# Kernel tuning notes

Measured on AMD Instinct MI355X. Metric: run time of the kernel, lower is better.

Reference implementation:

```python
import jax, jax.numpy as jnp
import numpy as np

D_MODEL = 768
NHEAD = 12
DK = D_MODEL // NHEAD
MAX_DIST = 1000.0
FF = 3072
POS_HIDDEN = 32  # hidden width of the relative-position bias MLP
EPS = 1e-5
B, L = 2, 1024


def setup_inputs() -> dict:
    key = jax.random.key(0)
    ks = jax.random.split(key, 24)

    def lin(k, i, o):  # torch-Linear-like init, stored as (in, out)
        return jax.random.uniform(k, (i, o), jnp.float32, -1.0, 1.0) / np.sqrt(i)

    return {
        "src": jax.random.normal(ks[0], (B, L, D_MODEL), jnp.float32),
        "src_x": jax.random.uniform(ks[1], (B, L), jnp.float32) * 1000.0,
        "src_y": jax.random.uniform(ks[2], (B, L), jnp.float32) * 1000.0,
        # attention projections (q,k,v,out)
        "Wq": lin(ks[3], D_MODEL, D_MODEL), "bq": jnp.zeros((D_MODEL,), jnp.float32),
        "Wk": lin(ks[4], D_MODEL, D_MODEL), "bk": jnp.zeros((D_MODEL,), jnp.float32),
        "Wv": lin(ks[5], D_MODEL, D_MODEL), "bv": jnp.zeros((D_MODEL,), jnp.float32),
        "Wo": lin(ks[6], D_MODEL, D_MODEL), "bo": jnp.zeros((D_MODEL,), jnp.float32),
        # relative-position bias MLP: 2 -> POS_HIDDEN -> NHEAD
        "P1": lin(ks[7], 2, POS_HIDDEN), "pb1": jnp.zeros((POS_HIDDEN,), jnp.float32),
        "P2": lin(ks[8], POS_HIDDEN, NHEAD), "pb2": jnp.zeros((NHEAD,), jnp.float32),
        # FFN
        "W1": lin(ks[9], D_MODEL, FF), "b1": jnp.zeros((FF,), jnp.float32),
        "W2": lin(ks[10], FF, D_MODEL), "b2": jnp.zeros((D_MODEL,), jnp.float32),
        # post-LN params
        "g1": jnp.ones((D_MODEL,), jnp.float32), "be1": jnp.zeros((D_MODEL,), jnp.float32),
        "g2": jnp.ones((D_MODEL,), jnp.float32), "be2": jnp.zeros((D_MODEL,), jnp.float32),
    }


def _layernorm(x, g, b):
    m = jnp.mean(x, axis=-1, keepdims=True)
    v = jnp.var(x, axis=-1, keepdims=True)
    return (x - m) * jax.lax.rsqrt(v + EPS) * g + b


def reference(src, src_x, src_y, Wq, bq, Wk, bk, Wv, bv, Wo, bo,
              P1, pb1, P2, pb2, W1, b1, W2, b2, g1, be1, g2, be2):
    b, l, _ = src.shape
    # projections -> (b, h, l, dk)
    q = (src @ Wq + bq).reshape(b, l, NHEAD, DK).transpose(0, 2, 1, 3)
    k = (src @ Wk + bk).reshape(b, l, NHEAD, DK).transpose(0, 2, 1, 3)
    v = (src @ Wv + bv).reshape(b, l, NHEAD, DK).transpose(0, 2, 1, 3)
    # 2D relative positions, clipped and normalized to [-1, 1]
    rx = jnp.clip(src_x[:, :, None] - src_x[:, None, :], -MAX_DIST, MAX_DIST) / MAX_DIST
    ry = jnp.clip(src_y[:, :, None] - src_y[:, None, :], -MAX_DIST, MAX_DIST) / MAX_DIST
    rel = jnp.stack([rx, ry], axis=-1)                        # (b, l, l, 2)
    bias = jax.nn.relu(rel @ P1 + pb1) @ P2 + pb2             # (b, l, l, h)
    bias = bias.transpose(0, 3, 1, 2)                         # (b, h, l, l)
    scores = jnp.einsum('bhqd,bhkd->bhqk', q, k) / np.sqrt(DK).astype(np.float32) + bias
    attn = jax.nn.softmax(scores, axis=-1)
    o = jnp.einsum('bhqk,bhkd->bhqd', attn, v).transpose(0, 2, 1, 3).reshape(b, l, D_MODEL)
    src2 = o @ Wo + bo
    x = _layernorm(src + src2, g1, be1)                       # post-LN residual 1
    ff = jax.nn.relu(x @ W1 + b1) @ W2 + b2                   # FFN
    return _layernorm(x + ff, g2, be2)                        # post-LN residual 2
```

## Files before the change

kernel.cpp:

```cpp
#include <hip/hip_runtime.h>
#include <math.h>

typedef unsigned short ushort_t;
typedef __attribute__((ext_vector_type(8))) short bf16x8;
typedef __attribute__((ext_vector_type(4))) float f32x4;

constexpr int kD      = 768;
constexpr int kNH     = 12;
constexpr int kDK     = 64;
constexpr int kFF     = 3072;
constexpr int kL      = 1024;
constexpr int kRows   = 2048;
constexpr float kEPS  = 1e-5f;
constexpr int kMLRows = 24 * kL;

__device__ __forceinline__ ushort_t f2bf(float f) {
    union { float f; unsigned u; } v; v.f = f;
    unsigned r = (v.u + 0x7fffu + ((v.u >> 16) & 1u)) >> 16;
    return (ushort_t)r;
}
__device__ __forceinline__ float bf2f(ushort_t u) {
    union { unsigned u; float f; } v; v.u = ((unsigned)u) << 16; return v.f;
}

#define GL_LDS(gp, lp) __builtin_amdgcn_global_load_lds( \
    (const __attribute__((address_space(1))) void*)(gp), \
    (__attribute__((address_space(3))) void*)(lp), 16, 0, 0)

template<int RELU, int OUTBF, int ADDBIAS>
__device__ __forceinline__ void gemm_body(const ushort_t* __restrict__ A,
                                          const ushort_t* __restrict__ WT,
                                          const float* __restrict__ bias,
                                          void* __restrict__ Cout,
                                          int N, int K, int row0, int col0,
                                          int kbeg, int kend)
{
    __shared__ ushort_t lds[8192];
    ushort_t* As = lds;
    ushort_t* Bs = lds + 4096;

    const int tid  = threadIdx.x;
    const int lane = tid & 63;
    const int wave = tid >> 6;
    const int wrow = (wave & 1) * 64;
    const int wcol = (wave >> 1) * 64;

    const int srow = wave * 16 + (lane >> 2);
    const int sk   = (lane & 3) * 8;
    const ushort_t* ga0 = A  + (size_t)(row0 + srow)      * K + sk;
    const ushort_t* ga1 = A  + (size_t)(row0 + srow + 64) * K + sk;
    const ushort_t* gb0 = WT + (size_t)(col0 + srow)      * K + sk;
    const ushort_t* gb1 = WT + (size_t)(col0 + srow + 64) * K + sk;
    ushort_t* la0 = As + wave * 512;
    ushort_t* la1 = As + 2048 + wave * 512;
    ushort_t* lb0 = Bs + wave * 512;
    ushort_t* lb1 = Bs + 2048 + wave * 512;

    const int fl = lane & 15, fq = lane >> 4;
    const ushort_t* fa[4];
    const ushort_t* fb[4];
    #pragma unroll
    for (int i = 0; i < 4; ++i) {
        fa[i] = As + (wrow + i * 16 + fl) * 32 + fq * 8;
        fb[i] = Bs + (wcol + i * 16 + fl) * 32 + fq * 8;
    }

    f32x4 acc[4][4] = {};

    for (int k0 = kbeg; k0 < kend; k0 += 32) {
        __syncthreads();
        GL_LDS(ga0 + k0, la0);
        GL_LDS(ga1 + k0, la1);
        GL_LDS(gb0 + k0, lb0);
        GL_LDS(gb1 + k0, lb1);
        __syncthreads();

        bf16x8 av[4], bv[4];
        #pragma unroll
        for (int i = 0; i < 4; ++i) {
            av[i] = *(const bf16x8*)fa[i];
            bv[i] = *(const bf16x8*)fb[i];
        }
        #pragma unroll
        for (int mi = 0; mi < 4; ++mi)
            #pragma unroll
            for (int ni = 0; ni < 4; ++ni)
                acc[mi][ni] = __builtin_amdgcn_mfma_f32_16x16x32_bf16(
                    av[mi], bv[ni], acc[mi][ni], 0, 0, 0);
    }

    #pragma unroll
    for (int mi = 0; mi < 4; ++mi) {
        const int m = wrow + mi * 16 + fq * 4;
        #pragma unroll
        for (int ni = 0; ni < 4; ++ni) {
            const int n = wcol + ni * 16 + fl;
            const float bb = ADDBIAS ? bias[col0 + n] : 0.f;
            #pragma unroll
            for (int r = 0; r < 4; ++r) {
                float v = acc[mi][ni][r] + bb;
                if (RELU) v = fmaxf(v, 0.f);
                const size_t idx = (size_t)(row0 + m + r) * N + col0 + n;
                if (OUTBF) ((ushort_t*)Cout)[idx] = f2bf(v);
                else       ((float*)Cout)[idx]    = v;
            }
        }
    }
}

template<int RELU, int OUTBF>
__global__ __launch_bounds__(256)
void gemm_kernel(const ushort_t* __restrict__ A, const ushort_t* __restrict__ WT,
                 const float* __restrict__ bias, void* __restrict__ Cout,
                 int N, int K)
{
    gemm_body<RELU, OUTBF, 1>(A, WT, bias, Cout, N, K,
                              blockIdx.y * 128, blockIdx.x * 128, 0, K);
}

__global__ __launch_bounds__(256)
void gemm_splitk_kernel(const ushort_t* __restrict__ A, const ushort_t* __restrict__ WT,
                        float* __restrict__ parts, int N, int K, int kslice)
{
    const int z = blockIdx.z;
    float* out = parts + (size_t)z * kRows * N;
    gemm_body<0, 0, 0>(A, WT, nullptr, out, N, K,
                       blockIdx.y * 128, blockIdx.x * 128, z * kslice, (z + 1) * kslice);
}

__global__ __launch_bounds__(256)
void gemm_qkv_kernel(const ushort_t* __restrict__ A,
                     const ushort_t* wq, const ushort_t* wk, const ushort_t* wv,
                     const float* bq, const float* bk, const float* bv,
                     ushort_t* q, ushort_t* k, ushort_t* v)
{
    const ushort_t* WT; const float* bias; ushort_t* out;
    if (blockIdx.z == 0)      { WT = wq; bias = bq; out = q; }
    else if (blockIdx.z == 1) { WT = wk; bias = bk; out = k; }
    else                      { WT = wv; bias = bv; out = v; }
    gemm_body<0, 1, 1>(A, WT, bias, out, kD, kD,
                       blockIdx.y * 128, blockIdx.x * 128, 0, kD);
}

struct WtDesc { const float* src; ushort_t* dst; int K; int N; };
struct WtArgs { WtDesc d[3]; };

__global__ __launch_bounds__(256)
void wt_kernel(WtArgs args)
{
    const WtDesc w = args.d[blockIdx.z];
    const int ktiles = w.K >> 6;
    const int kt = (blockIdx.x % ktiles) * 64;
    const int nt = (blockIdx.x / ktiles) * 64;
    if (nt >= w.N) return;

    __shared__ float T[64][65];
    const int tid = threadIdx.x;
    #pragma unroll
    for (int i = 0; i < 4; ++i) {
        const int e = tid + i * 256;
        const int r = e >> 4;
        const int c = (e & 15) * 4;
        const float4 f = *(const float4*)&w.src[(size_t)(kt + r) * w.N + nt + c];
        T[c + 0][r] = f.x; T[c + 1][r] = f.y; T[c + 2][r] = f.z; T[c + 3][r] = f.w;
    }
    __syncthreads();
    #pragma unroll
    for (int i = 0; i < 4; ++i) {
        const int e = tid + i * 256;
        const int n = e >> 4;
        const int kc = (e & 15) * 4;
        ushort4 o;
        o.x = f2bf(T[n][kc + 0]); o.y = f2bf(T[n][kc + 1]);
        o.z = f2bf(T[n][kc + 2]); o.w = f2bf(T[n][kc + 3]);
        *(ushort4*)&w.dst[(size_t)(nt + n) * w.K + kt + kc] = o;
    }
}

__global__ __launch_bounds__(256)
void cvt_kernel(const float* __restrict__ in, ushort_t* __restrict__ out, int n4)
{
    const int i = blockIdx.x * 256 + threadIdx.x;
    if (i < n4) {
        const float4 f = ((const float4*)in)[i];
        ushort4 o;
        o.x = f2bf(f.x); o.y = f2bf(f.y); o.z = f2bf(f.z); o.w = f2bf(f.w);
        ((ushort4*)out)[i] = o;
    }
}

__global__ __launch_bounds__(256)
void vtrans_kernel(const ushort_t* __restrict__ vb, ushort_t* __restrict__ vt)
{
    const int bh = blockIdx.x;
    const int b = bh / kNH, h = bh - b * kNH;
    const int j0 = blockIdx.y * 64;
    __shared__ ushort_t T[64][72];

    const int tid = threadIdx.x;
    {
        const int jr = tid & 63;
        const int c0 = (tid >> 6) * 16;
        const ushort_t* sp = vb + (size_t)(b * kL + j0 + jr) * kD + h * kDK + c0;
        uint4 u0 = *(const uint4*)sp;
        uint4 u1 = *(const uint4*)(sp + 8);
        const ushort_t* e0 = (const ushort_t*)&u0;
        const ushort_t* e1 = (const ushort_t*)&u1;
        #pragma unroll
        for (int jj = 0; jj < 8; ++jj) {
            T[c0 + jj][jr]     = e0[jj];
            T[c0 + 8 + jj][jr] = e1[jj];
        }
    }
    __syncthreads();
    {
        const int dr = tid >> 2;
        const int jc = (tid & 3) * 16;
        ushort_t* dp = vt + (size_t)(bh * 64 + dr) * kL + j0 + jc;
        *(uint4*)dp       = *(const uint4*)&T[dr][jc];
        *(uint4*)(dp + 8) = *(const uint4*)&T[dr][jc + 8];
    }
}

__global__ __launch_bounds__(256, 4)
void bias_kernel(const float* __restrict__ sx, const float* __restrict__ sy,
                 const float* __restrict__ P1, const float* __restrict__ pb1,
                 const float* __restrict__ P2, const float* __restrict__ pb2,
                 ushort_t* __restrict__ biasb)
{
    const int bid = blockIdx.x;
    const int b  = bid >> 10;
    const int qt = (bid >> 4) & 63;
    const int kt = bid & 15;
    const int tid = threadIdx.x;

    __shared__ float P[32][16];
    __shared__ float pb2l[12];
    __shared__ float qxl[16], qyl[16], kxl[64], kyl[64];
    __shared__ ushort_t Btile[12 * 1024];

    if (tid < 32) {
        P[tid][0] = P1[tid];
        P[tid][1] = P1[32 + tid];
        P[tid][2] = pb1[tid];
        P[tid][3] = 0.f;
    }
    for (int e = tid; e < 384; e += 256) P[e / 12][4 + e % 12] = P2[e];
    if (tid < 12) pb2l[tid] = pb2[tid];
    if (tid < 16) { qxl[tid] = sx[b * kL + qt * 16 + tid];
                    qyl[tid] = sy[b * kL + qt * 16 + tid]; }
    if (tid < 64) { kxl[tid] = sx[b * kL + kt * 64 + tid];
                    kyl[tid] = sy[b * kL + kt * 64 + tid]; }
    __syncthreads();

    const int ri = tid >> 4;
    const int fl = tid & 15;
    const int fq = ri >> 2, r = ri & 3;
    const int lane16 = fq * 16 + fl;
    const float xi = qxl[ri], yi = qyl[ri];

    float rx[4], ry[4];
    #pragma unroll
    for (int n = 0; n < 4; ++n) {
        const int cj = n * 16 + fl;
        rx[n] = fminf(fmaxf(xi - kxl[cj], -1000.f), 1000.f) * 1e-3f;
        ry[n] = fminf(fmaxf(yi - kyl[cj], -1000.f), 1000.f) * 1e-3f;
    }

    float acc[4][12] = {};
    #pragma unroll 4
    for (int u = 0; u < 32; ++u) {
        const float4 pc = *(const float4*)&P[u][0];
        const float4 w0 = *(const float4*)&P[u][4];
        const float4 w1 = *(const float4*)&P[u][8];
        const float4 w2 = *(const float4*)&P[u][12];
        float t[4];
        #pragma unroll
        for (int n = 0; n < 4; ++n)
            t[n] = fmaxf(fmaf(rx[n], pc.x, fmaf(ry[n], pc.y, pc.z)), 0.f);
        #pragma unroll
        for (int n = 0; n < 4; ++n) {
            acc[n][0]  = fmaf(t[n], w0.x, acc[n][0]);
            acc[n][1]  = fmaf(t[n], w0.y, acc[n][1]);
            acc[n][2]  = fmaf(t[n], w0.z, acc[n][2]);
            acc[n][3]  = fmaf(t[n], w0.w, acc[n][3]);
            acc[n][4]  = fmaf(t[n], w1.x, acc[n][4]);
            acc[n][5]  = fmaf(t[n], w1.y, acc[n][5]);
            acc[n][6]  = fmaf(t[n], w1.z, acc[n][6]);
            acc[n][7]  = fmaf(t[n], w1.w, acc[n][7]);
            acc[n][8]  = fmaf(t[n], w2.x, acc[n][8]);
            acc[n][9]  = fmaf(t[n], w2.y, acc[n][9]);
            acc[n][10] = fmaf(t[n], w2.z, acc[n][10]);
            acc[n][11] = fmaf(t[n], w2.w, acc[n][11]);
        }
    }

    #pragma unroll
    for (int h = 0; h < 12; ++h) {
        const float pb = pb2l[h];
        #pragma unroll
        for (int n = 0; n < 4; ++n)
            Btile[h * 1024 + lane16 * 16 + n * 4 + r] = f2bf(acc[n][h] + pb);
    }
    __syncthreads();

    #pragma unroll
    for (int i = 0; i < 6; ++i) {
        const int off = (i * 256 + tid) * 8;
        const int h = off >> 10;
        const int inner = off & 1023;
        ushort_t* dst = biasb +
            (((size_t)(b * kNH + h) * 64 + qt) * 16 + kt) * 1024 + inner;
        *(uint4*)dst = *(const uint4*)&Btile[off];
    }
}

__global__ __launch_bounds__(64, 3)
void attn_kernel(const ushort_t* __restrict__ qg, const ushort_t* __restrict__ kg,
                 const ushort_t* __restrict__ vt, const ushort_t* __restrict__ biasb,
                 ushort_t* __restrict__ p0, ushort_t* __restrict__ p1,
                 ushort_t* __restrict__ p2, ushort_t* __restrict__ p3,
                 float2* __restrict__ ml)
{
    const int bh = blockIdx.x;
    const int b  = bh / kNH, h = bh - b * kNH;
    const int qt = blockIdx.y;
    const int q0 = qt * 16;
    const int z  = blockIdx.z;
    const int lane = threadIdx.x;
    const int fl = lane & 15, fq = lane >> 4;

    __shared__ ushort_t Sp[16][72];

    const size_t qoff = (size_t)(b * kL + q0 + fl) * kD + h * kDK + fq * 8;
    const bf16x8 aq0 = *(const bf16x8*)(qg + qoff);
    const bf16x8 aq1 = *(const bf16x8*)(qg + qoff + 32);

    const ushort_t* kbase = kg + (size_t)(b * kL) * kD + h * kDK + fq * 8;
    const ushort_t* vbase = vt + (size_t)(bh * 64) * kL + fq * 8;
    const ushort_t* btile = biasb +
        ((size_t)(bh * 64 + qt) * 16 + z * 4) * 1024 + lane * 16;

    f32x4 accO[4] = {};
    float m_run[4] = {-INFINITY, -INFINITY, -INFINITY, -INFINITY};
    float l_run[4] = {};

    bf16x8 kc[4][2];
    uint4 bc0, bc1;
    {
        const int k0 = z * 256;
        #pragma unroll
        for (int n = 0; n < 4; ++n) {
            const ushort_t* kr = kbase + (size_t)(k0 + n * 16 + fl) * kD;
            kc[n][0] = *(const bf16x8*)kr;
            kc[n][1] = *(const bf16x8*)(kr + 32);
        }
        bc0 = *(const uint4*)btile;
        bc1 = *(const uint4*)(btile + 8);
    }

    #pragma unroll
    for (int t = 0; t < 4; ++t) {
        const int k0 = z * 256 + t * 64;

        bf16x8 vv[4][2];
        #pragma unroll
        for (int n = 0; n < 4; ++n) {
            const ushort_t* vr = vbase + (size_t)(n * 16 + fl) * kL + k0;
            vv[n][0] = *(const bf16x8*)vr;
            vv[n][1] = *(const bf16x8*)(vr + 32);
        }

        f32x4 S[4] = {};
        #pragma unroll
        for (int n = 0; n < 4; ++n) {
            S[n] = __builtin_amdgcn_mfma_f32_16x16x32_bf16(aq0, kc[n][0], S[n], 0, 0, 0);
            S[n] = __builtin_amdgcn_mfma_f32_16x16x32_bf16(aq1, kc[n][1], S[n], 0, 0, 0);
        }

        bf16x8 kn[4][2];
        uint4 bn0, bn1;
        if (t < 3) {
            #pragma unroll
            for (int n = 0; n < 4; ++n) {
                const ushort_t* kr = kbase + (size_t)(k0 + 64 + n * 16 + fl) * kD;
                kn[n][0] = *(const bf16x8*)kr;
                kn[n][1] = *(const bf16x8*)(kr + 32);
            }
            bn0 = *(const uint4*)(btile + (t + 1) * 1024);
            bn1 = *(const uint4*)(btile + (t + 1) * 1024 + 8);
        }

        ushort_t bu[16];
        *(uint4*)&bu[0] = bc0;
        *(uint4*)&bu[8] = bc1;
        #pragma unroll
        for (int n = 0; n < 4; ++n)
            #pragma unroll
            for (int r = 0; r < 4; ++r)
                S[n][r] = fmaf(S[n][r], 0.125f, bf2f(bu[n * 4 + r]));

        #pragma unroll
        for (int r = 0; r < 4; ++r) {
            float mx = fmaxf(fmaxf(S[0][r], S[1][r]), fmaxf(S[2][r], S[3][r]));
            mx = fmaxf(mx, __shfl_xor(mx, 1, 16));
            mx = fmaxf(mx, __shfl_xor(mx, 2, 16));
            mx = fmaxf(mx, __shfl_xor(mx, 4, 16));
            mx = fmaxf(mx, __shfl_xor(mx, 8, 16));
            const float mnew  = fmaxf(m_run[r], mx);
            const float alpha = __expf(m_run[r] - mnew);
            float ls = 0.f;
            #pragma unroll
            for (int n = 0; n < 4; ++n) {
                const float e = __expf(S[n][r] - mnew);
                S[n][r] = e;
                ls += e;
            }
            ls += __shfl_xor(ls, 1, 16);
            ls += __shfl_xor(ls, 2, 16);
            ls += __shfl_xor(ls, 4, 16);
            ls += __shfl_xor(ls, 8, 16);
            l_run[r] = l_run[r] * alpha + ls;
            m_run[r] = mnew;
            #pragma unroll
            for (int n = 0; n < 4; ++n) accO[n][r] *= alpha;
        }

        #pragma unroll
        for (int n = 0; n < 4; ++n)
            #pragma unroll
            for (int r = 0; r < 4; ++r)
                Sp[fq * 4 + r][n * 16 + fl] = f2bf(S[n][r]);
        __syncthreads();

        const bf16x8 ap0 = *(const bf16x8*)&Sp[fl][fq * 8];
        const bf16x8 ap1 = *(const bf16x8*)&Sp[fl][32 + fq * 8];
        #pragma unroll
        for (int n = 0; n < 4; ++n) {
            accO[n] = __builtin_amdgcn_mfma_f32_16x16x32_bf16(ap0, vv[n][0], accO[n], 0, 0, 0);
            accO[n] = __builtin_amdgcn_mfma_f32_16x16x32_bf16(ap1, vv[n][1], accO[n], 0, 0, 0);
        }
        __syncthreads();

        if (t < 3) {
            #pragma unroll
            for (int n = 0; n < 4; ++n) { kc[n][0] = kn[n][0]; kc[n][1] = kn[n][1]; }
            bc0 = bn0; bc1 = bn1;
        }
    }

    ushort_t* p = (z == 0) ? p0 : (z == 1) ? p1 : (z == 2) ? p2 : p3;
    float inv[4];
    #pragma unroll
    for (int r = 0; r < 4; ++r) inv[r] = 1.0f / l_run[r];
    #pragma unroll
    for (int n = 0; n < 4; ++n)
        #pragma unroll
        for (int r = 0; r < 4; ++r)
            p[(size_t)(b * kL + q0 + fq * 4 + r) * kD + h * kDK + n * 16 + fl] =
                f2bf(accO[n][r] * inv[r]);
    if (fl == 0) {
        #pragma unroll
        for (int r = 0; r < 4; ++r)
            ml[(size_t)z * kMLRows + bh * kL + q0 + fq * 4 + r] =
                make_float2(m_run[r], l_run[r]);
    }
}

__global__ __launch_bounds__(256)
void attn_combine_kernel(const ushort_t* __restrict__ p0, const ushort_t* __restrict__ p1,
                         const ushort_t* __restrict__ p2, const ushort_t* __restrict__ p3,
                         const float2* __restrict__ ml, ushort_t* __restrict__ out)
{
    const int tid = threadIdx.x;
    const int R = blockIdx.x * 32 + (tid >> 3);
    const int bh = R >> 10, i = R & 1023;
    const int b = bh / kNH, h = bh - b * kNH;

    const float2 s0 = ml[bh * kL + i];
    const float2 s1 = ml[kMLRows + bh * kL + i];
    const float2 s2 = ml[2 * kMLRows + bh * kL + i];
    const float2 s3 = ml[3 * kMLRows + bh * kL + i];
    const float M  = fmaxf(fmaxf(s0.x, s1.x), fmaxf(s2.x, s3.x));
    const float w0 = __expf(s0.x - M) * s0.y;
    const float w1 = __expf(s1.x - M) * s1.y;
    const float w2 = __expf(s2.x - M) * s2.y;
    const float w3 = __expf(s3.x - M) * s3.y;
    const float inv = 1.0f / (w0 + w1 + w2 + w3);
    const float c0 = w0 * inv, c1 = w1 * inv, c2 = w2 * inv, c3 = w3 * inv;

    const size_t base = (size_t)(b * kL + i) * kD + h * kDK + (tid & 7) * 8;
    uint4 u0 = *(const uint4*)(p0 + base);
    uint4 u1 = *(const uint4*)(p1 + base);
    uint4 u2 = *(const uint4*)(p2 + base);
    uint4 u3 = *(const uint4*)(p3 + base);
    const ushort_t* e0 = (const ushort_t*)&u0;
    const ushort_t* e1 = (const ushort_t*)&u1;
    const ushort_t* e2 = (const ushort_t*)&u2;
    const ushort_t* e3 = (const ushort_t*)&u3;
    ushort_t o[8];
    #pragma unroll
    for (int j = 0; j < 8; ++j)
        o[j] = f2bf(fmaf(c0, bf2f(e0[j]), fmaf(c1, bf2f(e1[j]),
                    fmaf(c2, bf2f(e2[j]), c3 * bf2f(e3[j])))));
    *(uint4*)(out + base) = *(const uint4*)o;
}

template<int NPART, int DUAL>
__global__ __launch_bounds__(256)
void ln_kernel(const float* __restrict__ a, const float* __restrict__ parts,
               const float* __restrict__ bias,
               const float* __restrict__ g, const float* __restrict__ be,
               float* __restrict__ out, ushort_t* __restrict__ out_bf)
{
    const int row = blockIdx.x;
    const int tid = threadIdx.x;
    const float* pa = a + (size_t)row * kD;
    constexpr size_t NTOK = (size_t)kRows * kD;

    float v[3];
    float s = 0.f, sq = 0.f;
    #pragma unroll
    for (int i = 0; i < 3; ++i) {
        const int d = tid + i * 256;
        float t = pa[d] + bias[d];
        #pragma unroll
        for (int p = 0; p < NPART; ++p)
            t += parts[p * NTOK + (size_t)row * kD + d];
        v[i] = t;
        s  += t;
        sq += t * t;
    }
    #pragma unroll
    for (int off = 32; off > 0; off >>= 1) {
        s  += __shfl_down(s, off);
        sq += __shfl_down(sq, off);
    }
    __shared__ float bs[4], bq2[4];
    if ((tid & 63) == 0) { bs[tid >> 6] = s; bq2[tid >> 6] = sq; }
    __syncthreads();
    const float ts = bs[0] + bs[1] + bs[2] + bs[3];
    const float tq = bq2[0] + bq2[1] + bq2[2] + bq2[3];
    const float invn = 1.0f / (float)kD;
    const float mean = ts * invn;
    const float var  = tq * invn - mean * mean;
    const float rstd = rsqrtf(var + kEPS);

    float* po = out + (size_t)row * kD;
    #pragma unroll
    for (int i = 0; i < 3; ++i) {
        const int d = tid + i * 256;
        const float o = (v[i] - mean) * rstd * g[d] + be[d];
        po[d] = o;
        if (DUAL) out_bf[(size_t)row * kD + d] = f2bf(o);
    }
}

extern "C" void kernel_launch(void* const* d_in, const int* in_sizes, int n_in,
                              void* d_out, int out_size, void* d_ws, size_t ws_size,
                              hipStream_t stream)
{
    const float* src = (const float*)d_in[0];
    const float* sx  = (const float*)d_in[1];
    const float* sy  = (const float*)d_in[2];
    const float* Wq  = (const float*)d_in[3];  const float* bq  = (const float*)d_in[4];
    const float* Wk  = (const float*)d_in[5];  const float* bk  = (const float*)d_in[6];
    const float* Wv  = (const float*)d_in[7];  const float* bv  = (const float*)d_in[8];
    const float* Wo  = (const float*)d_in[9];  const float* bo  = (const float*)d_in[10];
    const float* P1  = (const float*)d_in[11]; const float* pb1 = (const float*)d_in[12];
    const float* P2  = (const float*)d_in[13]; const float* pb2 = (const float*)d_in[14];
    const float* W1  = (const float*)d_in[15]; const float* b1  = (const float*)d_in[16];
    const float* W2  = (const float*)d_in[17]; const float* b2  = (const float*)d_in[18];
    const float* g1  = (const float*)d_in[19]; const float* be1 = (const float*)d_in[20];
    const float* g2  = (const float*)d_in[21]; const float* be2 = (const float*)d_in[22];

    constexpr size_t W768  = 768u * 768u;
    constexpr size_t W3072 = 768u * 3072u;
    constexpr size_t NTOK  = (size_t)kRows * kD;

    ushort_t* wsu = (ushort_t*)d_ws;
    ushort_t* wqT = wsu;
    ushort_t* wkT = wqT + W768;
    ushort_t* wvT = wkT + W768;
    ushort_t* qb  = wvT + W768;
    ushort_t* kb  = qb + NTOK;
    ushort_t* vb  = kb + NTOK;
    ushort_t* sb  = vb + NTOK;
    ushort_t* vtb = sb + NTOK;
    ushort_t* biasb = vtb + NTOK;
    ushort_t* woT   = biasb;
    ushort_t* w1T   = woT + W768;
    ushort_t* w2T   = w1T + W3072;
    float*    xb    = (float*)(w2T + W3072);
    ushort_t* h1bf  = (ushort_t*)(xb + NTOK);
    float*    s2p   = (float*)h1bf;
    float*    ff2p  = (float*)(h1bf + 4 * NTOK);
    float2*   mlb   = (float2*)wqT;
    ushort_t* p2b   = (ushort_t*)d_out;
    ushort_t* p3b   = p2b + NTOK;
    ushort_t* xbf   = qb;

    const dim3 blk(256);

    WtArgs wa_early;
    wa_early.d[0] = { Wq, wqT, kD, kD };
    wa_early.d[1] = { Wk, wkT, kD, kD };
    wa_early.d[2] = { Wv, wvT, kD, kD };
    wt_kernel<<<dim3(144, 1, 3), blk, 0, stream>>>(wa_early);
    cvt_kernel<<<dim3((int)(NTOK / 4 / 256)), blk, 0, stream>>>(src, sb, (int)(NTOK / 4));
    bias_kernel<<<dim3(2048), blk, 0, stream>>>(sx, sy, P1, pb1, P2, pb2, biasb);

    gemm_qkv_kernel<<<dim3(kD / 128, kRows / 128, 3), blk, 0, stream>>>(
        sb, wqT, wkT, wvT, bq, bk, bv, qb, kb, vb);

    vtrans_kernel<<<dim3(2 * kNH, kL / 64), blk, 0, stream>>>(vb, vtb);

    attn_kernel<<<dim3(2 * kNH, kL / 16, 4), dim3(64), 0, stream>>>(
        qb, kb, vtb, biasb, sb, vb, p2b, p3b, mlb);
    attn_combine_kernel<<<dim3(768), blk, 0, stream>>>(sb, vb, p2b, p3b, mlb, qb);

    WtArgs wa_late;
    wa_late.d[0] = { Wo, woT, kD,  kD  };
    wa_late.d[1] = { W1, w1T, kD,  kFF };
    wa_late.d[2] = { W2, w2T, kFF, kD  };
    wt_kernel<<<dim3(576, 1, 3), blk, 0, stream>>>(wa_late);

    gemm_splitk_kernel<<<dim3(kD / 128, kRows / 128, 2), blk, 0, stream>>>(
        qb, woT, s2p, kD, kD, kD / 2);

    ln_kernel<2, 1><<<dim3(kRows), blk, 0, stream>>>(src, s2p, bo, g1, be1, xb, xbf);

    gemm_kernel<1, 1><<<dim3(kFF / 128, kRows / 128), blk, 0, stream>>>(
        xbf, w1T, b1, h1bf, kFF, kD);

    gemm_splitk_kernel<<<dim3(kD / 128, kRows / 128, 3), blk, 0, stream>>>(
        h1bf, w2T, ff2p, kD, kFF, kFF / 3);

    ln_kernel<3, 0><<<dim3(kRows), blk, 0, stream>>>(xb, ff2p, b2, g2, be2,
                                                     (float*)d_out, nullptr);
}
```

Before: 313.0 us.

## Fuse split-KV attention partial combine into attention kernel via LDS

Instead of launching four separate 64-thread blocks per query tile that write bf16 partial outputs and (m,l) stats to global memory, each 256-thread block now runs the four KV splits as four waves and merges them in shared memory. The separate combine kernel launch and the global round-trip of the partials are removed. The per-iteration block-wide barriers are dropped since each wave uses its own Sp slice. The larger block with more LDS may reduce how many blocks fit per CU.

```diff
diff --git a/kernel.cpp b/kernel.cpp
--- a/kernel.cpp
+++ b/kernel.cpp
@@ -12,7 +12,6 @@
 constexpr int kL      = 1024;
 constexpr int kRows   = 2048;
 constexpr float kEPS  = 1e-5f;
-constexpr int kMLRows = 24 * kL;
 
 __device__ __forceinline__ ushort_t f2bf(float f) {
     union { float f; unsigned u; } v; v.f = f;
@@ -315,22 +314,23 @@
     }
 }
 
-__global__ __launch_bounds__(64, 3)
+__global__ __launch_bounds__(256)
 void attn_kernel(const ushort_t* __restrict__ qg, const ushort_t* __restrict__ kg,
                  const ushort_t* __restrict__ vt, const ushort_t* __restrict__ biasb,
-                 ushort_t* __restrict__ p0, ushort_t* __restrict__ p1,
-                 ushort_t* __restrict__ p2, ushort_t* __restrict__ p3,
-                 float2* __restrict__ ml)
+                 ushort_t* __restrict__ og)
 {
     const int bh = blockIdx.x;
     const int b  = bh / kNH, h = bh - b * kNH;
     const int qt = blockIdx.y;
     const int q0 = qt * 16;
-    const int z  = blockIdx.z;
-    const int lane = threadIdx.x;
+    const int tid = threadIdx.x;
+    const int z  = tid >> 6;
+    const int lane = tid & 63;
     const int fl = lane & 15, fq = lane >> 4;
 
-    __shared__ ushort_t Sp[16][72];
+    __shared__ ushort_t Sp[4][16][72];
+    __shared__ ushort_t Ob[4][16][64];
+    __shared__ float2   Ml[4][16];
 
     const size_t qoff = (size_t)(b * kL + q0 + fl) * kD + h * kDK + fq * 8;
     const bf16x8 aq0 = *(const bf16x8*)(qg + qoff);
@@ -430,17 +430,15 @@
         for (int n = 0; n < 4; ++n)
             #pragma unroll
             for (int r = 0; r < 4; ++r)
-                Sp[fq * 4 + r][n * 16 + fl] = f2bf(S[n][r]);
-        __syncthreads();
-
-        const bf16x8 ap0 = *(const bf16x8*)&Sp[fl][fq * 8];
-        const bf16x8 ap1 = *(const bf16x8*)&Sp[fl][32 + fq * 8];
+                Sp[z][fq * 4 + r][n * 16 + fl] = f2bf(S[n][r]);
+
+        const bf16x8 ap0 = *(const bf16x8*)&Sp[z][fl][fq * 8];
+        const bf16x8 ap1 = *(const bf16x8*)&Sp[z][fl][32 + fq * 8];
         #pragma unroll
         for (int n = 0; n < 4; ++n) {
             accO[n] = __builtin_amdgcn_mfma_f32_16x16x32_bf16(ap0, vv[n][0], accO[n], 0, 0, 0);
             accO[n] = __builtin_amdgcn_mfma_f32_16x16x32_bf16(ap1, vv[n][1], accO[n], 0, 0, 0);
         }
-        __syncthreads();
 
         if (t < 3) {
             #pragma unroll
@@ -449,7 +447,6 @@
         }
     }
 
-    ushort_t* p = (z == 0) ? p0 : (z == 1) ? p1 : (z == 2) ? p2 : p3;
     float inv[4];
     #pragma unroll
     for (int r = 0; r < 4; ++r) inv[r] = 1.0f / l_run[r];
@@ -457,53 +454,35 @@
     for (int n = 0; n < 4; ++n)
         #pragma unroll
         for (int r = 0; r < 4; ++r)
-            p[(size_t)(b * kL + q0 + fq * 4 + r) * kD + h * kDK + n * 16 + fl] =
-                f2bf(accO[n][r] * inv[r]);
+            Ob[z][fq * 4 + r][n * 16 + fl] = f2bf(accO[n][r] * inv[r]);
     if (fl == 0) {
         #pragma unroll
         for (int r = 0; r < 4; ++r)
-            ml[(size_t)z * kMLRows + bh * kL + q0 + fq * 4 + r] =
-                make_float2(m_run[r], l_run[r]);
-    }
-}
-
-__global__ __launch_bounds__(256)
-void attn_combine_kernel(const ushort_t* __restrict__ p0, const ushort_t* __restrict__ p1,
-                         const ushort_t* __restrict__ p2, const ushort_t* __restrict__ p3,
-                         const float2* __restrict__ ml, ushort_t* __restrict__ out)
-{
-    const int tid = threadIdx.x;
-    const int R = blockIdx.x * 32 + (tid >> 3);
-    const int bh = R >> 10, i = R & 1023;
-    const int b = bh / kNH, h = bh - b * kNH;
-
-    const float2 s0 = ml[bh * kL + i];
-    const float2 s1 = ml[kMLRows + bh * kL + i];
-    const float2 s2 = ml[2 * kMLRows + bh * kL + i];
-    const float2 s3 = ml[3 * kMLRows + bh * kL + i];
-    const float M  = fmaxf(fmaxf(s0.x, s1.x), fmaxf(s2.x, s3.x));
-    const float w0 = __expf(s0.x - M) * s0.y;
-    const float w1 = __expf(s1.x - M) * s1.y;
-    const float w2 = __expf(s2.x - M) * s2.y;
-    const float w3 = __expf(s3.x - M) * s3.y;
-    const float inv = 1.0f / (w0 + w1 + w2 + w3);
-    const float c0 = w0 * inv, c1 = w1 * inv, c2 = w2 * inv, c3 = w3 * inv;
-
-    const size_t base = (size_t)(b * kL + i) * kD + h * kDK + (tid & 7) * 8;
-    uint4 u0 = *(const uint4*)(p0 + base);
-    uint4 u1 = *(const uint4*)(p1 + base);
-    uint4 u2 = *(const uint4*)(p2 + base);
-    uint4 u3 = *(const uint4*)(p3 + base);
-    const ushort_t* e0 = (const ushort_t*)&u0;
-    const ushort_t* e1 = (const ushort_t*)&u1;
-    const ushort_t* e2 = (const ushort_t*)&u2;
-    const ushort_t* e3 = (const ushort_t*)&u3;
-    ushort_t o[8];
-    #pragma unroll
-    for (int j = 0; j < 8; ++j)
-        o[j] = f2bf(fmaf(c0, bf2f(e0[j]), fmaf(c1, bf2f(e1[j]),
-                    fmaf(c2, bf2f(e2[j]), c3 * bf2f(e3[j])))));
-    *(uint4*)(out + base) = *(const uint4*)o;
+            Ml[z][fq * 4 + r] = make_float2(m_run[r], l_run[r]);
+    }
+    __syncthreads();
+
+    {
+        const int ri = tid >> 4;
+        const int d0 = (tid & 15) * 4;
+        const float2 s0 = Ml[0][ri], s1 = Ml[1][ri], s2 = Ml[2][ri], s3 = Ml[3][ri];
+        const float M = fmaxf(fmaxf(s0.x, s1.x), fmaxf(s2.x, s3.x));
+        const float w0 = __expf(s0.x - M) * s0.y;
+        const float w1 = __expf(s1.x - M) * s1.y;
+        const float w2 = __expf(s2.x - M) * s2.y;
+        const float w3 = __expf(s3.x - M) * s3.y;
+        const float winv = 1.0f / (w0 + w1 + w2 + w3);
+        const float c0 = w0 * winv, c1 = w1 * winv, c2 = w2 * winv, c3 = w3 * winv;
+
+        ushort_t o[4];
+        #pragma unroll
+        for (int j = 0; j < 4; ++j)
+            o[j] = f2bf(fmaf(c0, bf2f(Ob[0][ri][d0 + j]),
+                        fmaf(c1, bf2f(Ob[1][ri][d0 + j]),
+                        fmaf(c2, bf2f(Ob[2][ri][d0 + j]),
+                             c3 * bf2f(Ob[3][ri][d0 + j])))));
+        *(uint2*)&og[(size_t)(b * kL + q0 + ri) * kD + h * kDK + d0] = *(const uint2*)o;
+    }
 }
 
 template<int NPART, int DUAL>
@@ -595,9 +574,6 @@
     ushort_t* h1bf  = (ushort_t*)(xb + NTOK);
     float*    s2p   = (float*)h1bf;
     float*    ff2p  = (float*)(h1bf + 4 * NTOK);
-    float2*   mlb   = (float2*)wqT;
-    ushort_t* p2b   = (ushort_t*)d_out;
-    ushort_t* p3b   = p2b + NTOK;
     ushort_t* xbf   = qb;
 
     const dim3 blk(256);
@@ -615,9 +591,7 @@
 
     vtrans_kernel<<<dim3(2 * kNH, kL / 64), blk, 0, stream>>>(vb, vtb);
 
-    attn_kernel<<<dim3(2 * kNH, kL / 16, 4), dim3(64), 0, stream>>>(
-        qb, kb, vtb, biasb, sb, vb, p2b, p3b, mlb);
-    attn_combine_kernel<<<dim3(768), blk, 0, stream>>>(sb, vb, p2b, p3b, mlb, qb);
+    attn_kernel<<<dim3(2 * kNH, kL / 16), blk, 0, stream>>>(qb, kb, vtb, biasb, sb);
 
     WtArgs wa_late;
     wa_late.d[0] = { Wo, woT, kD,  kD  };
@@ -626,7 +600,7 @@
     wt_kernel<<<dim3(576, 1, 3), blk, 0, stream>>>(wa_late);
 
     gemm_splitk_kernel<<<dim3(kD / 128, kRows / 128, 2), blk, 0, stream>>>(
-        qb, woT, s2p, kD, kD, kD / 2);
+        sb, woT, s2p, kD, kD, kD / 2);
 
     ln_kernel<2, 1><<<dim3(kRows), blk, 0, stream>>>(src, s2p, bo, g1, be1, xb, xbf);
 
```

Result: faster. 298.6 us (-4.6%).
